# Kernel tuning notes

Hardware: AMD Instinct MI355X
Metric: run time of the kernel (lower is better)

## Reference

```python
import jax, jax.numpy as jnp
import numpy as np

N_A, N_C, N_L = 50000, 10000, 10000
HID = 128


def _gatv2(x_src, x_dst, src, dst, ea, Wl, bl, Wr, br, We, att, bias, H):
    # GATv2Conv (PyG) bipartite, edge_dim=1, concat=False (mean over heads), eval mode (no dropout)
    C = bias.shape[0]
    n_dst = x_dst.shape[0]
    xl = (x_src @ Wl + bl).reshape(-1, H, C)      # [N_src, H, C]
    xr = (x_dst @ Wr + br).reshape(-1, H, C)      # [N_dst, H, C]
    e = jax.nn.leaky_relu(xl[src] + xr[dst] + (ea @ We).reshape(-1, H, C), 0.2)  # [E,H,C]
    logit = jnp.einsum('ehc,hc->eh', e, att)      # [E,H]
    m = jax.ops.segment_max(logit, dst, num_segments=n_dst)
    m = jax.lax.stop_gradient(jnp.where(jnp.isfinite(m), m, 0.0))
    ex = jnp.exp(logit - m[dst])
    denom = jax.ops.segment_sum(ex, dst, num_segments=n_dst)
    alpha = ex / (denom[dst] + 1e-16)             # segment softmax over incoming edges
    out = jax.ops.segment_sum(alpha[:, :, None] * xl[src], dst, num_segments=n_dst)
    return out.mean(axis=1) + bias                # concat=False -> head mean + bias


def setup_inputs() -> dict:
    key = jax.random.key(0)
    ks = iter(jax.random.split(key, 80))
    def rn(shape, s=1.0):
        return jax.random.normal(next(ks), shape, jnp.float32) * s
    inp = {}
    inp['x_asset'] = rn((N_A, 512))
    inp['x_creator'] = rn((N_C, 2))
    inp['x_licensee'] = rn((N_L, 1))
    # edges: (name, E, src_max, dst_max)
    edges = [('cb', 50000, N_A, N_C), ('lt', 100000, N_A, N_L), ('sim', 200000, N_A, N_A),
             ('fw', 100000, N_A, N_A), ('rcb', 50000, N_C, N_A), ('rlt', 100000, N_L, N_A)]
    for name, E, smax, dmax in edges:
        inp[f'{name}_src'] = jax.random.randint(next(ks), (E,), 0, smax, jnp.int32)
        inp[f'{name}_dst'] = jax.random.randint(next(ks), (E,), 0, dmax, jnp.int32)
        inp[f'ea_{name}'] = rn((E, 1))
    w = 0.05  # param scale
    inp['Wp_a'] = rn((512, HID), w); inp['bp_a'] = rn((HID,), w)
    inp['Wp_c'] = rn((2, HID), w);   inp['bp_c'] = rn((HID,), w)
    inp['Wp_l'] = rn((1, HID), w);   inp['bp_l'] = rn((HID,), w)
    # layer 1: heads=2, stacked over the 6 relations
    H1 = 2
    inp['Wl1'] = rn((6, HID, H1 * HID), w); inp['bl1'] = rn((6, H1 * HID), w)
    inp['Wr1'] = rn((6, HID, H1 * HID), w); inp['br1'] = rn((6, H1 * HID), w)
    inp['We1'] = rn((6, 1, H1 * HID), w)
    inp['att1'] = rn((6, H1, HID), w); inp['bias1'] = rn((6, HID), w)
    # layer 2: heads=1
    inp['Wl2'] = rn((6, HID, HID), w); inp['bl2'] = rn((6, HID), w)
    inp['Wr2'] = rn((6, HID, HID), w); inp['br2'] = rn((6, HID), w)
    inp['We2'] = rn((6, 1, HID), w)
    inp['att2'] = rn((6, 1, HID), w); inp['bias2'] = rn((6, HID), w)
    inp['Wc1'] = rn((HID, HID), w); inp['bc1'] = rn((HID,), w)
    inp['Wc2'] = rn((HID, 3), w);   inp['bc2'] = rn((3,), w)
    inp['query_asset_index'] = 123
    return inp


def reference(x_asset, x_creator, x_licensee, Wp_a, bp_a, Wp_c, bp_c, Wp_l, bp_l,
              Wl1, bl1, Wr1, br1, We1, att1, bias1,
              Wl2, bl2, Wr2, br2, We2, att2, bias2,
              Wc1, bc1, Wc2, bc2,
              ea_cb, ea_lt, ea_sim, ea_fw, ea_rcb, ea_rlt,
              cb_src, cb_dst, lt_src, lt_dst, sim_src, sim_dst,
              fw_src, fw_dst, rcb_src, rcb_dst, rlt_src, rlt_dst,
              query_asset_index):
    x = {'Asset': x_asset @ Wp_a + bp_a,
         'Creator': x_creator @ Wp_c + bp_c,
         'Licensee': x_licensee @ Wp_l + bp_l}
    rels = [('Asset', 'Creator', cb_src, cb_dst, ea_cb),
            ('Asset', 'Licensee', lt_src, lt_dst, ea_lt),
            ('Asset', 'Asset', sim_src, sim_dst, ea_sim),
            ('Asset', 'Asset', fw_src, fw_dst, ea_fw),
            ('Creator', 'Asset', rcb_src, rcb_dst, ea_rcb),
            ('Licensee', 'Asset', rlt_src, rlt_dst, ea_rlt)]

    def hetero_layer(x, Wl, bl, Wr, br, We, att, bias, H):
        out = {k: jnp.zeros((v.shape[0], HID), v.dtype) for k, v in x.items()}
        for i, (st, dt, s, d, ea) in enumerate(rels):  # HeteroConv aggr='sum'
            out[dt] = out[dt] + _gatv2(x[st], x[dt], s, d, ea,
                                       Wl[i], bl[i], Wr[i], br[i], We[i], att[i], bias[i], H)
        return out

    x = hetero_layer(x, Wl1, bl1, Wr1, br1, We1, att1, bias1, 2)
    x = {k: jax.nn.relu(v) for k, v in x.items()}  # eval: dropout is identity
    x = hetero_layer(x, Wl2, bl2, Wr2, br2, We2, att2, bias2, 1)
    x = {k: jax.nn.relu(v) for k, v in x.items()}
    a = x['Asset'][query_asset_index]
    return jax.nn.relu(a @ Wc1 + bc1) @ Wc2 + bc2
```

## Files before the change

### kernel.cpp

```cpp
#include <hip/hip_runtime.h>
#include <math.h>

#define FAMAX 64
#define FCMAX 32
#define FLMAX 32
#define PAMAX 256
#define PCMAX 64
#define PLMAX 64
#define N1MAX 512
#define N2MAX 128

struct Inputs {
  const float *x_asset, *x_creator, *x_licensee;
  const float *Wp_a,*bp_a,*Wp_c,*bp_c,*Wp_l,*bp_l;
  const float *Wl1,*bl1,*Wr1,*br1,*We1,*att1,*bias1;
  const float *Wl2,*bl2,*Wr2,*br2,*We2,*att2,*bias2;
  const float *Wc1,*bc1,*Wc2,*bc2;
};

struct Edges {
  const int *cb_s,*cb_d;  const float* ea_cb;  int Ecb;
  const int *lt_s,*lt_d;  const float* ea_lt;  int Elt;
  const int *sim_s,*sim_d;const float* ea_sim; int Esim;
  const int *fw_s,*fw_d;  const float* ea_fw;  int Efw;
  const int *rcb_s,*rcb_d;const float* ea_rcb; int Ercb;
  const int *rlt_s,*rlt_d;const float* ea_rlt; int Erlt;
};

struct WSP {
  int* cnt;
  int *dfA,*dfC,*dfL;
  int *pfA,*pfC,*pfL;
  int *fa,*fc,*fl;
  int *pa,*pc,*pl;
  int* l2rel; int* l2src; float* l2ea;
  int* l1rel; int* l1src; int* l1dslot; float* l1ea;
  float *h0a,*h0c,*h0l;
  float *xr1a,*xr1c,*xr1l;
  float* xl1e;
  float* logit1;
  float *x1a,*x1c,*x1l;
  float* xr2q;
  float* xl2e;
  float* logit2;
};

__device__ __forceinline__ float leaky(float x){ return x > 0.f ? x : 0.2f*x; }

__device__ __forceinline__ void claim(int* flag, int* cnt, int* list, int node, int cap){
  int old = atomicCAS(&flag[node], 0, 1);
  if (old == 0){
    int k = atomicAdd(cnt, 1);
    if (k < cap){ list[k] = node; atomicExch(&flag[node], k + 2); }
    else atomicExch(&flag[node], 0);
  }
}

__global__ void k1_scan_l2(Edges eg, const int* qptr, WSP w){
  int q = qptr[0];
  if (blockIdx.x==0 && threadIdx.x==0){
    claim(w.dfA, &w.cnt[1], w.fa, q, FAMAX);
    claim(w.pfA, &w.cnt[5], w.pa, q, PAMAX);
  }
  int total = eg.Esim + eg.Efw + eg.Ercb + eg.Erlt;
  for (int i = blockIdx.x*blockDim.x + threadIdx.x; i < total; i += gridDim.x*blockDim.x){
    int j = i, rel; const int *sp,*dp; const float* ep;
    if (j < eg.Esim){ rel=2; sp=eg.sim_s; dp=eg.sim_d; ep=eg.ea_sim; }
    else { j -= eg.Esim;
      if (j < eg.Efw){ rel=3; sp=eg.fw_s; dp=eg.fw_d; ep=eg.ea_fw; }
      else { j -= eg.Efw;
        if (j < eg.Ercb){ rel=4; sp=eg.rcb_s; dp=eg.rcb_d; ep=eg.ea_rcb; }
        else { j -= eg.Ercb; rel=5; sp=eg.rlt_s; dp=eg.rlt_d; ep=eg.ea_rlt; }
      }
    }
    if (dp[j] == q){
      int src = sp[j];
      int k = atomicAdd(&w.cnt[0], 1);
      if (k < N2MAX){ w.l2rel[k]=rel; w.l2src[k]=src; w.l2ea[k]=ep[j]; }
      if (rel <= 3){ claim(w.dfA,&w.cnt[1],w.fa,src,FAMAX); claim(w.pfA,&w.cnt[5],w.pa,src,PAMAX); }
      else if (rel == 4){ claim(w.dfC,&w.cnt[2],w.fc,src,FCMAX); claim(w.pfC,&w.cnt[6],w.pc,src,PCMAX); }
      else { claim(w.dfL,&w.cnt[3],w.fl,src,FLMAX); claim(w.pfL,&w.cnt[7],w.pl,src,PLMAX); }
    }
  }
}

__global__ void k2_scan_l1(Edges eg, WSP w){
  int total = eg.Ecb+eg.Elt+eg.Esim+eg.Efw+eg.Ercb+eg.Erlt;
  for (int i = blockIdx.x*blockDim.x + threadIdx.x; i < total; i += gridDim.x*blockDim.x){
    int j = i, rel; const int *sp,*dp; const float* ep; const int* flag;
    if (j < eg.Ecb){ rel=0; sp=eg.cb_s; dp=eg.cb_d; ep=eg.ea_cb; flag=w.dfC; }
    else { j -= eg.Ecb;
    if (j < eg.Elt){ rel=1; sp=eg.lt_s; dp=eg.lt_d; ep=eg.ea_lt; flag=w.dfL; }
    else { j -= eg.Elt;
    if (j < eg.Esim){ rel=2; sp=eg.sim_s; dp=eg.sim_d; ep=eg.ea_sim; flag=w.dfA; }
    else { j -= eg.Esim;
    if (j < eg.Efw){ rel=3; sp=eg.fw_s; dp=eg.fw_d; ep=eg.ea_fw; flag=w.dfA; }
    else { j -= eg.Efw;
    if (j < eg.Ercb){ rel=4; sp=eg.rcb_s; dp=eg.rcb_d; ep=eg.ea_rcb; flag=w.dfA; }
    else { j -= eg.Ercb; rel=5; sp=eg.rlt_s; dp=eg.rlt_d; ep=eg.ea_rlt; flag=w.dfA; }}}}}
    int f = flag[dp[j]];
    if (f >= 2){
      int src = sp[j];
      int k = atomicAdd(&w.cnt[4], 1);
      if (k < N1MAX){ w.l1rel[k]=rel; w.l1src[k]=src; w.l1dslot[k]=f-2; w.l1ea[k]=ep[j]; }
      if (rel <= 3) claim(w.pfA,&w.cnt[5],w.pa,src,PAMAX);
      else if (rel == 4) claim(w.pfC,&w.cnt[6],w.pc,src,PCMAX);
      else claim(w.pfL,&w.cnt[7],w.pl,src,PLMAX);
    }
  }
}

__global__ void k3a_proj(Inputs in, WSP w){
  int b = blockIdx.x, t = threadIdx.x;
  if (b < PAMAX){
    __shared__ float xs[512];
    __shared__ float part[512];
    int npa = w.cnt[5] < PAMAX ? w.cnt[5] : PAMAX;
    if (b >= npa) return;
    int node = w.pa[b];
    xs[t] = in.x_asset[(size_t)node*512 + t];
    __syncthreads();
    int j = t & 127, g = t >> 7;
    float acc = 0.f;
    const float* W = in.Wp_a + (size_t)g*128*128 + j;
    const float* xg = xs + g*128;
    for (int k=0;k<128;k++) acc = fmaf(xg[k], W[(size_t)k*128], acc);
    part[t] = acc;
    __syncthreads();
    if (t < 128)
      w.h0a[(size_t)b*128 + t] = in.bp_a[t] + part[t] + part[128+t] + part[256+t] + part[384+t];
  } else if (b == PAMAX){
    int npc = w.cnt[6] < PCMAX ? w.cnt[6] : PCMAX;
    int j = t & 127, s0 = t >> 7;
    for (int s = s0; s < npc; s += 4){
      int node = w.pc[s];
      w.h0c[s*128 + j] = in.bp_c[j] + in.x_creator[node*2]*in.Wp_c[j]
                       + in.x_creator[node*2+1]*in.Wp_c[128+j];
    }
  } else {
    int npl = w.cnt[7] < PLMAX ? w.cnt[7] : PLMAX;
    int j = t & 127, s0 = t >> 7;
    for (int s = s0; s < npl; s += 4){
      int node = w.pl[s];
      w.h0l[s*128 + j] = in.bp_l[j] + in.x_licensee[node]*in.Wp_l[j];
    }
  }
}

__global__ void k3b_xr1(Inputs in, WSP w){
  __shared__ float h0[128];
  int b = blockIdx.x, t = threadIdx.x;
  int rel; const float* hsrc; float* dst;
  if (b < FAMAX*4){
    int slot = b >> 2, ridx = b & 3;
    int nfa = w.cnt[1] < FAMAX ? w.cnt[1] : FAMAX;
    if (slot >= nfa) return;
    rel = 2 + ridx;
    int ps = w.pfA[w.fa[slot]] - 2; if (ps < 0) return;
    hsrc = w.h0a + (size_t)ps*128;
    dst = w.xr1a + ((size_t)slot*4 + ridx)*256;
  } else if (b < FAMAX*4 + FCMAX){
    int slot = b - FAMAX*4;
    int nfc = w.cnt[2] < FCMAX ? w.cnt[2] : FCMAX;
    if (slot >= nfc) return;
    rel = 0;
    int ps = w.pfC[w.fc[slot]] - 2; if (ps < 0) return;
    hsrc = w.h0c + (size_t)ps*128;
    dst = w.xr1c + (size_t)slot*256;
  } else {
    int slot = b - FAMAX*4 - FCMAX;
    int nfl = w.cnt[3] < FLMAX ? w.cnt[3] : FLMAX;
    if (slot >= nfl) return;
    rel = 1;
    int ps = w.pfL[w.fl[slot]] - 2; if (ps < 0) return;
    hsrc = w.h0l + (size_t)ps*128;
    dst = w.xr1l + (size_t)slot*256;
  }
  if (t < 128) h0[t] = hsrc[t];
  __syncthreads();
  float acc = in.br1[rel*256 + t];
  const float* W = in.Wr1 + (size_t)rel*128*256 + t;
  for (int c=0;c<128;c++) acc = fmaf(h0[c], W[(size_t)c*256], acc);
  dst[t] = acc;
}

__global__ void k3c_edge(Inputs in, WSP w){
  __shared__ float h0[128];
  __shared__ float red[256];
  int i = blockIdx.x, t = threadIdx.x;
  int n1 = w.cnt[4] < N1MAX ? w.cnt[4] : N1MAX;
  if (i >= n1) return;
  int rel = w.l1rel[i], src = w.l1src[i], dslot = w.l1dslot[i];
  float ea = w.l1ea[i];
  int ps; const float* hsrc;
  if (rel <= 3){ ps = w.pfA[src]-2; hsrc = w.h0a + (size_t)(ps>0?ps:0)*128; }
  else if (rel == 4){ ps = w.pfC[src]-2; hsrc = w.h0c + (size_t)(ps>0?ps:0)*128; }
  else { ps = w.pfL[src]-2; hsrc = w.h0l + (size_t)(ps>0?ps:0)*128; }
  if (ps < 0){
    w.xl1e[(size_t)i*256 + t] = 0.f;
    if (t < 2) w.logit1[i*2 + t] = -INFINITY;
    return;
  }
  if (t < 128) h0[t] = hsrc[t];
  __syncthreads();
  float acc = in.bl1[rel*256 + t];
  const float* W = in.Wl1 + (size_t)rel*128*256 + t;
  for (int c=0;c<128;c++) acc = fmaf(h0[c], W[(size_t)c*256], acc);
  w.xl1e[(size_t)i*256 + t] = acc;
  const float* xr;
  if (rel >= 2) xr = w.xr1a + ((size_t)dslot*4 + (rel-2))*256;
  else if (rel == 0) xr = w.xr1c + (size_t)dslot*256;
  else xr = w.xr1l + (size_t)dslot*256;
  int h = t >> 7, c = t & 127;
  float e = leaky(acc + xr[t] + ea*in.We1[rel*256 + t]);
  red[t] = e * in.att1[(rel*2 + h)*128 + c];
  __syncthreads();
  for (int s=64; s>0; s>>=1){ if (c < s) red[t] += red[t+s]; __syncthreads(); }
  if (c == 0) w.logit1[i*2 + h] = red[t];
}

__global__ void k4_agg(Inputs in, WSP w){
  int b = blockIdx.x, j = threadIdx.x;
  int nfa = w.cnt[1] < FAMAX ? w.cnt[1] : FAMAX;
  int nfc = w.cnt[2] < FCMAX ? w.cnt[2] : FCMAX;
  int nfl = w.cnt[3] < FLMAX ? w.cnt[3] : FLMAX;
  int type, slot;
  if (b < FAMAX){ slot=b; if (slot>=nfa) return; type=0; }
  else if (b < FAMAX+FCMAX){ slot=b-FAMAX; if (slot>=nfc) return; type=1; }
  else { slot=b-FAMAX-FCMAX; if (slot>=nfl) return; type=2; }
  int n1 = w.cnt[4] < N1MAX ? w.cnt[4] : N1MAX;
  float out = 0.f;
  int r0, r1;
  if (type==0){ r0=2; r1=5; } else if (type==1){ r0=0; r1=0; } else { r0=1; r1=1; }
  for (int r=r0; r<=r1; r++){
    out += in.bias1[r*128 + j];
    float m0=-INFINITY, m1=-INFINITY;
    for (int i=0;i<n1;i++){
      if (w.l1rel[i]==r && w.l1dslot[i]==slot){
        m0 = fmaxf(m0, w.logit1[i*2]);
        m1 = fmaxf(m1, w.logit1[i*2+1]);
      }
    }
    if (m0 == -INFINITY) continue;
    float d0=0.f, d1=0.f, a0=0.f, a1=0.f;
    for (int i=0;i<n1;i++){
      if (w.l1rel[i]==r && w.l1dslot[i]==slot){
        float e0 = expf(w.logit1[i*2]   - m0);
        float e1 = expf(w.logit1[i*2+1] - m1);
        d0 += e0; d1 += e1;
        a0 = fmaf(e0, w.xl1e[(size_t)i*256 + j],       a0);
        a1 = fmaf(e1, w.xl1e[(size_t)i*256 + 128 + j], a1);
      }
    }
    out += 0.5f*(a0/(d0+1e-16f) + a1/(d1+1e-16f));
  }
  float v = fmaxf(out, 0.f);
  if (type==0) w.x1a[slot*128 + j] = v;
  else if (type==1) w.x1c[slot*128 + j] = v;
  else w.x1l[slot*128 + j] = v;
}

__global__ void k5a_xr2(Inputs in, WSP w, const int* qptr){
  __shared__ float xq[128];
  int t = threadIdx.x;
  int q = qptr[0];
  int qs = w.dfA[q] - 2;
  if (t < 128) xq[t] = w.x1a[(size_t)qs*128 + t];
  __syncthreads();
  int ridx = t >> 7, j = t & 127;
  int r = 2 + ridx;
  float acc = in.br2[r*128 + j];
  const float* W = in.Wr2 + (size_t)r*128*128 + j;
  for (int c=0;c<128;c++) acc = fmaf(xq[c], W[(size_t)c*128], acc);
  w.xr2q[ridx*128 + j] = acc;
}

__global__ void k5b_l2edge(Inputs in, WSP w){
  __shared__ float xs[128];
  __shared__ float red[128];
  int i = blockIdx.x, j = threadIdx.x;
  int n2 = w.cnt[0] < N2MAX ? w.cnt[0] : N2MAX;
  if (i >= n2) return;
  int rel = w.l2rel[i], src = w.l2src[i];
  float ea = w.l2ea[i];
  int f; const float* xb;
  if (rel <= 3){ f = w.dfA[src]; xb = w.x1a; }
  else if (rel == 4){ f = w.dfC[src]; xb = w.x1c; }
  else { f = w.dfL[src]; xb = w.x1l; }
  if (f < 2){
    w.xl2e[(size_t)i*128 + j] = 0.f;
    if (j == 0) w.logit2[i] = -INFINITY;
    return;
  }
  xs[j] = xb[(size_t)(f-2)*128 + j];
  __syncthreads();
  float acc = in.bl2[rel*128 + j];
  const float* W = in.Wl2 + (size_t)rel*128*128 + j;
  for (int c=0;c<128;c++) acc = fmaf(xs[c], W[(size_t)c*128], acc);
  w.xl2e[(size_t)i*128 + j] = acc;
  float e = leaky(acc + w.xr2q[(rel-2)*128 + j] + ea*in.We2[rel*128 + j]);
  red[j] = e * in.att2[rel*128 + j];
  __syncthreads();
  for (int s=64; s>0; s>>=1){ if (j < s) red[j] += red[j+s]; __syncthreads(); }
  if (j == 0) w.logit2[i] = red[0];
}

__global__ void k5c_final(Inputs in, WSP w, float* outp){
  __shared__ float x2[128];
  __shared__ float tt[128];
  int j = threadIdx.x;
  int n2 = w.cnt[0] < N2MAX ? w.cnt[0] : N2MAX;
  float o = 0.f;
  for (int r=2; r<=5; r++){
    o += in.bias2[r*128 + j];
    float m = -INFINITY;
    for (int i=0;i<n2;i++) if (w.l2rel[i]==r) m = fmaxf(m, w.logit2[i]);
    if (m == -INFINITY) continue;
    float d = 0.f, acc = 0.f;
    for (int i=0;i<n2;i++) if (w.l2rel[i]==r){
      float e = expf(w.logit2[i] - m);
      d += e;
      acc = fmaf(e, w.xl2e[(size_t)i*128 + j], acc);
    }
    o += acc/(d + 1e-16f);
  }
  x2[j] = fmaxf(o, 0.f);
  __syncthreads();
  float acc = in.bc1[j];
  for (int c=0;c<128;c++) acc = fmaf(x2[c], in.Wc1[c*128 + j], acc);
  tt[j] = fmaxf(acc, 0.f);
  __syncthreads();
  if (j < 3){
    float r = in.bc2[j];
    for (int c=0;c<128;c++) r = fmaf(tt[c], in.Wc2[c*3 + j], r);
    outp[j] = r;
  }
}

extern "C" void kernel_launch(void* const* d_in, const int* in_sizes, int n_in,
                              void* d_out, int out_size, void* d_ws, size_t ws_size,
                              hipStream_t stream){
  Inputs in;
  in.x_asset   = (const float*)d_in[0];
  in.x_creator = (const float*)d_in[1];
  in.x_licensee= (const float*)d_in[2];
  Edges eg;
  eg.cb_s =(const int*)d_in[3];  eg.cb_d =(const int*)d_in[4];  eg.ea_cb =(const float*)d_in[5];  eg.Ecb = in_sizes[3];
  eg.lt_s =(const int*)d_in[6];  eg.lt_d =(const int*)d_in[7];  eg.ea_lt =(const float*)d_in[8];  eg.Elt = in_sizes[6];
  eg.sim_s=(const int*)d_in[9];  eg.sim_d=(const int*)d_in[10]; eg.ea_sim=(const float*)d_in[11]; eg.Esim= in_sizes[9];
  eg.fw_s =(const int*)d_in[12]; eg.fw_d =(const int*)d_in[13]; eg.ea_fw =(const float*)d_in[14]; eg.Efw = in_sizes[12];
  eg.rcb_s=(const int*)d_in[15]; eg.rcb_d=(const int*)d_in[16]; eg.ea_rcb=(const float*)d_in[17]; eg.Ercb= in_sizes[15];
  eg.rlt_s=(const int*)d_in[18]; eg.rlt_d=(const int*)d_in[19]; eg.ea_rlt=(const float*)d_in[20]; eg.Erlt= in_sizes[18];
  in.Wp_a=(const float*)d_in[21]; in.bp_a=(const float*)d_in[22];
  in.Wp_c=(const float*)d_in[23]; in.bp_c=(const float*)d_in[24];
  in.Wp_l=(const float*)d_in[25]; in.bp_l=(const float*)d_in[26];
  in.Wl1=(const float*)d_in[27]; in.bl1=(const float*)d_in[28];
  in.Wr1=(const float*)d_in[29]; in.br1=(const float*)d_in[30];
  in.We1=(const float*)d_in[31]; in.att1=(const float*)d_in[32]; in.bias1=(const float*)d_in[33];
  in.Wl2=(const float*)d_in[34]; in.bl2=(const float*)d_in[35];
  in.Wr2=(const float*)d_in[36]; in.br2=(const float*)d_in[37];
  in.We2=(const float*)d_in[38]; in.att2=(const float*)d_in[39]; in.bias2=(const float*)d_in[40];
  in.Wc1=(const float*)d_in[41]; in.bc1=(const float*)d_in[42];
  in.Wc2=(const float*)d_in[43]; in.bc2=(const float*)d_in[44];
  const int* qptr = (const int*)d_in[45];

  char* p = (char*)d_ws;
  auto carve = [&](size_t n)->char*{ char* r = p; p += ((n + 255) & ~(size_t)255); return r; };
  WSP w;
  w.cnt  = (int*)carve(16*4);
  w.dfA  = (int*)carve(50000*4); w.dfC = (int*)carve(10000*4); w.dfL = (int*)carve(10000*4);
  w.pfA  = (int*)carve(50000*4); w.pfC = (int*)carve(10000*4); w.pfL = (int*)carve(10000*4);
  size_t zero_bytes = (size_t)(p - (char*)d_ws);
  w.fa = (int*)carve(FAMAX*4); w.fc = (int*)carve(FCMAX*4); w.fl = (int*)carve(FLMAX*4);
  w.pa = (int*)carve(PAMAX*4); w.pc = (int*)carve(PCMAX*4); w.pl = (int*)carve(PLMAX*4);
  w.l2rel=(int*)carve(N2MAX*4); w.l2src=(int*)carve(N2MAX*4); w.l2ea=(float*)carve(N2MAX*4);
  w.l1rel=(int*)carve(N1MAX*4); w.l1src=(int*)carve(N1MAX*4); w.l1dslot=(int*)carve(N1MAX*4); w.l1ea=(float*)carve(N1MAX*4);
  w.h0a=(float*)carve((size_t)PAMAX*128*4);
  w.h0c=(float*)carve((size_t)PCMAX*128*4);
  w.h0l=(float*)carve((size_t)PLMAX*128*4);
  w.xr1a=(float*)carve((size_t)FAMAX*4*256*4);
  w.xr1c=(float*)carve((size_t)FCMAX*256*4);
  w.xr1l=(float*)carve((size_t)FLMAX*256*4);
  w.xl1e=(float*)carve((size_t)N1MAX*256*4);
  w.logit1=(float*)carve((size_t)N1MAX*2*4);
  w.x1a=(float*)carve((size_t)FAMAX*128*4);
  w.x1c=(float*)carve((size_t)FCMAX*128*4);
  w.x1l=(float*)carve((size_t)FLMAX*128*4);
  w.xr2q=(float*)carve(4*128*4);
  w.xl2e=(float*)carve((size_t)N2MAX*128*4);
  w.logit2=(float*)carve(N2MAX*4);

  hipMemsetAsync(d_ws, 0, zero_bytes, stream);

  int tE2 = eg.Esim + eg.Efw + eg.Ercb + eg.Erlt;
  k1_scan_l2<<<(tE2+255)/256, 256, 0, stream>>>(eg, qptr, w);
  int tE1 = eg.Ecb + eg.Elt + tE2;
  k2_scan_l1<<<(tE1+255)/256, 256, 0, stream>>>(eg, w);
  k3a_proj<<<PAMAX+2, 512, 0, stream>>>(in, w);
  k3b_xr1<<<FAMAX*4 + FCMAX + FLMAX, 256, 0, stream>>>(in, w);
  k3c_edge<<<N1MAX, 256, 0, stream>>>(in, w);
  k4_agg<<<FAMAX + FCMAX + FLMAX, 128, 0, stream>>>(in, w);
  k5a_xr2<<<1, 512, 0, stream>>>(in, w, qptr);
  k5b_l2edge<<<N2MAX, 128, 0, stream>>>(in, w);
  k5c_final<<<1, 128, 0, stream>>>(in, w, (float*)d_out);
}
```

Baseline: 309.6 us.

## Fuse all pipeline stages into one cooperative persistent kernel with grid syncs

Replaces the memset plus nine separate kernel launches with a single cooperative kernel of 512 blocks that runs every stage, separated by grid-wide barriers. Cross-block data is passed through relaxed agent-scope atomic loads and stores. The workspace zeroing also moves inside the kernel. The aim is to remove per-launch overhead and inter-kernel gaps in a latency-bound, tiny-work pipeline. The cost is grid.sync overhead, fixed parallelism and extra complexity; if the cooperative launch fails, the original multi-kernel path runs instead.

New measurement: 711.9 us. 2.3x slower.

```diff
diff --git a/kernel.cpp b/kernel.cpp
--- a/kernel.cpp
+++ b/kernel.cpp
@@ -1,5 +1,8 @@
 #include <hip/hip_runtime.h>
+#include <hip/hip_cooperative_groups.h>
 #include <math.h>
+
+namespace cg = cooperative_groups;
 
 #define FAMAX 64
 #define FCMAX 32
@@ -9,6 +12,10 @@
 #define PLMAX 64
 #define N1MAX 512
 #define N2MAX 128
+#define DMAX  64
+#define GRID  512
+#define BLK   256
+#define NZERO (16 + 50000 + 10000 + 10000 + 50000 + 10000 + 10000)
 
 struct Inputs {
   const float *x_asset, *x_creator, *x_licensee;
@@ -46,13 +53,346 @@
 };
 
 __device__ __forceinline__ float leaky(float x){ return x > 0.f ? x : 0.2f*x; }
+__device__ __forceinline__ int   ldi(const int* p){ return __hip_atomic_load(p, __ATOMIC_RELAXED, __HIP_MEMORY_SCOPE_AGENT); }
+__device__ __forceinline__ void  sti(int* p, int v){ __hip_atomic_store(p, v, __ATOMIC_RELAXED, __HIP_MEMORY_SCOPE_AGENT); }
+__device__ __forceinline__ float ldf(const float* p){ return __hip_atomic_load(p, __ATOMIC_RELAXED, __HIP_MEMORY_SCOPE_AGENT); }
+__device__ __forceinline__ void  stf(float* p, float v){ __hip_atomic_store(p, v, __ATOMIC_RELAXED, __HIP_MEMORY_SCOPE_AGENT); }
+__device__ __forceinline__ int   imin(int a,int b){ return a<b?a:b; }
 
 __device__ __forceinline__ void claim(int* flag, int* cnt, int* list, int node, int cap){
   int old = atomicCAS(&flag[node], 0, 1);
   if (old == 0){
     int k = atomicAdd(cnt, 1);
-    if (k < cap){ list[k] = node; atomicExch(&flag[node], k + 2); }
+    if (k < cap){ sti(list + k, node); atomicExch(&flag[node], k + 2); }
     else atomicExch(&flag[node], 0);
+  }
+}
+
+__global__ __launch_bounds__(BLK, 2)
+void mega(Inputs in, Edges eg, const int* qptr, WSP w, float* outp){
+  cg::grid_group g = cg::this_grid();
+  const int t = threadIdx.x;
+  const int gtid = blockIdx.x*BLK + t;
+  const int gstride = gridDim.x*BLK;
+
+  __shared__ float xs[512];
+  __shared__ float part[256];
+  __shared__ float h0[128];
+  __shared__ float red[256];
+  __shared__ int   lrel[N1MAX];
+  __shared__ int   lslot[N1MAX];
+  __shared__ float lea[N1MAX];
+  __shared__ float lg[DMAX][2];
+  __shared__ int   eid[DMAX];
+  __shared__ float lg2[N2MAX];
+  __shared__ int   srl2[N2MAX];
+  __shared__ float vx[128];
+
+  int* zbase = w.cnt;
+  for (int i = gtid; i < NZERO; i += gstride) sti(zbase + i, 0);
+  g.sync();
+
+  int q = qptr[0];
+  if (blockIdx.x == 0 && t == 0){
+    claim(w.dfA, &w.cnt[1], w.fa, q, FAMAX);
+    claim(w.pfA, &w.cnt[5], w.pa, q, PAMAX);
+  }
+  {
+    int total = eg.Esim + eg.Efw + eg.Ercb + eg.Erlt;
+    for (int i = gtid; i < total; i += gstride){
+      int j = i, rel; const int *sp,*dp; const float* ep;
+      if (j < eg.Esim){ rel=2; sp=eg.sim_s; dp=eg.sim_d; ep=eg.ea_sim; }
+      else { j -= eg.Esim;
+        if (j < eg.Efw){ rel=3; sp=eg.fw_s; dp=eg.fw_d; ep=eg.ea_fw; }
+        else { j -= eg.Efw;
+          if (j < eg.Ercb){ rel=4; sp=eg.rcb_s; dp=eg.rcb_d; ep=eg.ea_rcb; }
+          else { j -= eg.Ercb; rel=5; sp=eg.rlt_s; dp=eg.rlt_d; ep=eg.ea_rlt; }
+        }
+      }
+      if (dp[j] == q){
+        int src = sp[j];
+        int k = atomicAdd(&w.cnt[0], 1);
+        if (k < N2MAX){ sti(w.l2rel+k, rel); sti(w.l2src+k, src); stf(w.l2ea+k, ep[j]); }
+        if (rel <= 3){ claim(w.dfA,&w.cnt[1],w.fa,src,FAMAX); claim(w.pfA,&w.cnt[5],w.pa,src,PAMAX); }
+        else if (rel == 4){ claim(w.dfC,&w.cnt[2],w.fc,src,FCMAX); claim(w.pfC,&w.cnt[6],w.pc,src,PCMAX); }
+        else { claim(w.dfL,&w.cnt[3],w.fl,src,FLMAX); claim(w.pfL,&w.cnt[7],w.pl,src,PLMAX); }
+      }
+    }
+  }
+  g.sync();
+
+  {
+    int total = eg.Ecb+eg.Elt+eg.Esim+eg.Efw+eg.Ercb+eg.Erlt;
+    for (int i = gtid; i < total; i += gstride){
+      int j = i, rel; const int *sp,*dp; const float* ep; int* flag;
+      if (j < eg.Ecb){ rel=0; sp=eg.cb_s; dp=eg.cb_d; ep=eg.ea_cb; flag=w.dfC; }
+      else { j -= eg.Ecb;
+      if (j < eg.Elt){ rel=1; sp=eg.lt_s; dp=eg.lt_d; ep=eg.ea_lt; flag=w.dfL; }
+      else { j -= eg.Elt;
+      if (j < eg.Esim){ rel=2; sp=eg.sim_s; dp=eg.sim_d; ep=eg.ea_sim; flag=w.dfA; }
+      else { j -= eg.Esim;
+      if (j < eg.Efw){ rel=3; sp=eg.fw_s; dp=eg.fw_d; ep=eg.ea_fw; flag=w.dfA; }
+      else { j -= eg.Efw;
+      if (j < eg.Ercb){ rel=4; sp=eg.rcb_s; dp=eg.rcb_d; ep=eg.ea_rcb; flag=w.dfA; }
+      else { j -= eg.Ercb; rel=5; sp=eg.rlt_s; dp=eg.rlt_d; ep=eg.ea_rlt; flag=w.dfA; }}}}}
+      int f = ldi(&flag[dp[j]]);
+      if (f >= 2){
+        int src = sp[j];
+        int k = atomicAdd(&w.cnt[4], 1);
+        if (k < N1MAX){ sti(w.l1rel+k, rel); sti(w.l1src+k, src); sti(w.l1dslot+k, f-2); stf(w.l1ea+k, ep[j]); }
+        if (rel <= 3) claim(w.pfA,&w.cnt[5],w.pa,src,PAMAX);
+        else if (rel == 4) claim(w.pfC,&w.cnt[6],w.pc,src,PCMAX);
+        else claim(w.pfL,&w.cnt[7],w.pl,src,PLMAX);
+      }
+    }
+  }
+  g.sync();
+
+  {
+    int npa = imin(ldi(&w.cnt[5]), PAMAX);
+    int npc = imin(ldi(&w.cnt[6]), PCMAX);
+    int npl = imin(ldi(&w.cnt[7]), PLMAX);
+    for (int task = blockIdx.x; task < PAMAX + 2; task += gridDim.x){
+      if (task < PAMAX){
+        if (task >= npa) continue;
+        int node = ldi(w.pa + task);
+        xs[t]     = in.x_asset[(size_t)node*512 + t];
+        xs[t+256] = in.x_asset[(size_t)node*512 + t + 256];
+        __syncthreads();
+        int j = t & 127, g2 = t >> 7;
+        float acc = 0.f;
+        const float* W = in.Wp_a + (size_t)g2*256*128 + j;
+        const float* xg = xs + g2*256;
+        for (int k=0;k<256;k++) acc = fmaf(xg[k], W[(size_t)k*128], acc);
+        part[t] = acc;
+        __syncthreads();
+        if (t < 128) stf(w.h0a + (size_t)task*128 + t, in.bp_a[t] + part[t] + part[128+t]);
+        __syncthreads();
+      } else if (task == PAMAX){
+        int j = t & 127, s0 = t >> 7;
+        for (int s = s0; s < npc; s += 2){
+          int node = ldi(w.pc + s);
+          stf(w.h0c + s*128 + j, in.bp_c[j] + in.x_creator[node*2]*in.Wp_c[j]
+                                + in.x_creator[node*2+1]*in.Wp_c[128+j]);
+        }
+      } else {
+        int j = t & 127, s0 = t >> 7;
+        for (int s = s0; s < npl; s += 2){
+          int node = ldi(w.pl + s);
+          stf(w.h0l + s*128 + j, in.bp_l[j] + in.x_licensee[node]*in.Wp_l[j]);
+        }
+      }
+    }
+  }
+  g.sync();
+
+  {
+    int nfa = imin(ldi(&w.cnt[1]), FAMAX);
+    int nfc = imin(ldi(&w.cnt[2]), FCMAX);
+    int nfl = imin(ldi(&w.cnt[3]), FLMAX);
+    int n1  = imin(ldi(&w.cnt[4]), N1MAX);
+    int ntask = FAMAX*4 + FCMAX + FLMAX + n1;
+    for (int task = blockIdx.x; task < ntask; task += gridDim.x){
+      if (task < FAMAX*4 + FCMAX + FLMAX){
+        int rel; const float* hsrc; float* dst;
+        if (task < FAMAX*4){
+          int slot = task >> 2, ridx = task & 3;
+          if (slot >= nfa) continue;
+          rel = 2 + ridx;
+          int ps = ldi(&w.pfA[ldi(w.fa + slot)]) - 2; if (ps < 0) continue;
+          hsrc = w.h0a + (size_t)ps*128;
+          dst = w.xr1a + ((size_t)slot*4 + ridx)*256;
+        } else if (task < FAMAX*4 + FCMAX){
+          int slot = task - FAMAX*4;
+          if (slot >= nfc) continue;
+          rel = 0;
+          int ps = ldi(&w.pfC[ldi(w.fc + slot)]) - 2; if (ps < 0) continue;
+          hsrc = w.h0c + (size_t)ps*128;
+          dst = w.xr1c + (size_t)slot*256;
+        } else {
+          int slot = task - FAMAX*4 - FCMAX;
+          if (slot >= nfl) continue;
+          rel = 1;
+          int ps = ldi(&w.pfL[ldi(w.fl + slot)]) - 2; if (ps < 0) continue;
+          hsrc = w.h0l + (size_t)ps*128;
+          dst = w.xr1l + (size_t)slot*256;
+        }
+        if (t < 128) h0[t] = ldf(hsrc + t);
+        __syncthreads();
+        float acc = in.br1[rel*256 + t];
+        const float* W = in.Wr1 + (size_t)rel*128*256 + t;
+        for (int c=0;c<128;c++) acc = fmaf(h0[c], W[(size_t)c*256], acc);
+        stf(dst + t, acc);
+        __syncthreads();
+      } else {
+        int i = task - (FAMAX*4 + FCMAX + FLMAX);
+        int rel = ldi(w.l1rel + i), src = ldi(w.l1src + i);
+        int ps; const float* hsrc;
+        if (rel <= 3){ ps = ldi(&w.pfA[src]) - 2; hsrc = w.h0a + (size_t)(ps>0?ps:0)*128; }
+        else if (rel == 4){ ps = ldi(&w.pfC[src]) - 2; hsrc = w.h0c + (size_t)(ps>0?ps:0)*128; }
+        else { ps = ldi(&w.pfL[src]) - 2; hsrc = w.h0l + (size_t)(ps>0?ps:0)*128; }
+        if (ps < 0){ if (t == 0) sti(w.l1rel + i, -1); continue; }
+        if (t < 128) h0[t] = ldf(hsrc + t);
+        __syncthreads();
+        float acc = in.bl1[rel*256 + t];
+        const float* W = in.Wl1 + (size_t)rel*128*256 + t;
+        for (int c=0;c<128;c++) acc = fmaf(h0[c], W[(size_t)c*256], acc);
+        stf(w.xl1e + (size_t)i*256 + t, acc);
+        __syncthreads();
+      }
+    }
+  }
+  g.sync();
+
+  {
+    int nfa = imin(ldi(&w.cnt[1]), FAMAX);
+    int nfc = imin(ldi(&w.cnt[2]), FCMAX);
+    int nfl = imin(ldi(&w.cnt[3]), FLMAX);
+    int n1  = imin(ldi(&w.cnt[4]), N1MAX);
+    for (int task = blockIdx.x; task < FAMAX + FCMAX + FLMAX; task += gridDim.x){
+      int type, slot;
+      if (task < FAMAX){ slot=task; if (slot>=nfa) continue; type=0; }
+      else if (task < FAMAX+FCMAX){ slot=task-FAMAX; if (slot>=nfc) continue; type=1; }
+      else { slot=task-FAMAX-FCMAX; if (slot>=nfl) continue; type=2; }
+      for (int i = t; i < n1; i += BLK){
+        lrel[i] = ldi(w.l1rel + i); lslot[i] = ldi(w.l1dslot + i); lea[i] = ldf(w.l1ea + i);
+      }
+      __syncthreads();
+      int h = t >> 7, c = t & 127;
+      float out = 0.f;
+      int r0, r1;
+      if (type==0){ r0=2; r1=5; } else if (type==1){ r0=0; r1=0; } else { r0=1; r1=1; }
+      for (int r=r0; r<=r1; r++){
+        if (t < 128) out += in.bias1[r*128 + t];
+        const float* xrp;
+        if (r >= 2) xrp = w.xr1a + ((size_t)slot*4 + (r-2))*256;
+        else if (r == 0) xrp = w.xr1c + (size_t)slot*256;
+        else xrp = w.xr1l + (size_t)slot*256;
+        float xrv = ldf(xrp + t);
+        float wev = in.We1[r*256 + t];
+        float atv = in.att1[(r*2 + h)*128 + c];
+        int nd = 0;
+        for (int i=0;i<n1 && nd<DMAX;i++){
+          if (lrel[i]==r && lslot[i]==slot){
+            float e = leaky(ldf(w.xl1e + (size_t)i*256 + t) + xrv + lea[i]*wev);
+            red[t] = e * atv;
+            __syncthreads();
+            for (int s=64; s>0; s>>=1){ if (c < s) red[t] += red[t+s]; __syncthreads(); }
+            if (t == 0){ lg[nd][0] = red[0]; lg[nd][1] = red[128]; eid[nd] = i; }
+            __syncthreads();
+            nd++;
+          }
+        }
+        if (nd == 0) continue;
+        float m0=-INFINITY, m1=-INFINITY;
+        for (int d=0; d<nd; d++){ m0 = fmaxf(m0, lg[d][0]); m1 = fmaxf(m1, lg[d][1]); }
+        float d0=0.f, d1=0.f;
+        for (int d=0; d<nd; d++){ d0 += expf(lg[d][0]-m0); d1 += expf(lg[d][1]-m1); }
+        if (t < 128){
+          float a0=0.f, a1=0.f;
+          for (int d=0; d<nd; d++){
+            int i = eid[d];
+            a0 = fmaf(expf(lg[d][0]-m0), ldf(w.xl1e + (size_t)i*256 + t),       a0);
+            a1 = fmaf(expf(lg[d][1]-m1), ldf(w.xl1e + (size_t)i*256 + 128 + t), a1);
+          }
+          out += 0.5f*(a0/(d0+1e-16f) + a1/(d1+1e-16f));
+        }
+        __syncthreads();
+      }
+      if (t < 128){
+        float v = fmaxf(out, 0.f);
+        if (type==0) stf(w.x1a + slot*128 + t, v);
+        else if (type==1) stf(w.x1c + slot*128 + t, v);
+        else stf(w.x1l + slot*128 + t, v);
+      }
+      __syncthreads();
+    }
+  }
+  g.sync();
+
+  {
+    int n2 = imin(ldi(&w.cnt[0]), N2MAX);
+    for (int task = blockIdx.x; task < 1 + n2; task += gridDim.x){
+      if (task == 0){
+        int qs = ldi(&w.dfA[q]) - 2;
+        if (t < 128) h0[t] = ldf(w.x1a + (size_t)qs*128 + t);
+        __syncthreads();
+        int j = t & 127;
+        for (int rr = t >> 7; rr < 4; rr += 2){
+          int r = 2 + rr;
+          float acc = in.br2[r*128 + j];
+          const float* W = in.Wr2 + (size_t)r*128*128 + j;
+          for (int c=0;c<128;c++) acc = fmaf(h0[c], W[(size_t)c*128], acc);
+          stf(w.xr2q + rr*128 + j, acc);
+        }
+        __syncthreads();
+      } else {
+        int i = task - 1;
+        int rel = ldi(w.l2rel + i), src = ldi(w.l2src + i);
+        int f; const float* xb;
+        if (rel <= 3){ f = ldi(&w.dfA[src]); xb = w.x1a; }
+        else if (rel == 4){ f = ldi(&w.dfC[src]); xb = w.x1c; }
+        else { f = ldi(&w.dfL[src]); xb = w.x1l; }
+        if (f < 2){ if (t == 0) sti(w.l2rel + i, -1); continue; }
+        if (t < 128) h0[t] = ldf(xb + (size_t)(f-2)*128 + t);
+        __syncthreads();
+        if (t < 128){
+          float acc = in.bl2[rel*128 + t];
+          const float* W = in.Wl2 + (size_t)rel*128*128 + t;
+          for (int c=0;c<128;c++) acc = fmaf(h0[c], W[(size_t)c*128], acc);
+          stf(w.xl2e + (size_t)i*128 + t, acc);
+        }
+        __syncthreads();
+      }
+    }
+  }
+  g.sync();
+
+  if (blockIdx.x == 0){
+    int n2 = imin(ldi(&w.cnt[0]), N2MAX);
+    for (int i=0;i<n2;i++){
+      int rel = ldi(w.l2rel + i);
+      if (rel < 0){ if (t == 0) srl2[i] = -1; __syncthreads(); continue; }
+      float ea = ldf(w.l2ea + i);
+      if (t < 128){
+        float e = leaky(ldf(w.xl2e + (size_t)i*128 + t) + ldf(w.xr2q + (rel-2)*128 + t)
+                        + ea*in.We2[rel*128 + t]);
+        red[t] = e * in.att2[rel*128 + t];
+      }
+      __syncthreads();
+      for (int s=64; s>0; s>>=1){ if (t < s) red[t] += red[t+s]; __syncthreads(); }
+      if (t == 0){ lg2[i] = red[0]; srl2[i] = rel; }
+      __syncthreads();
+    }
+    float o = 0.f;
+    if (t < 128){
+      for (int r=2; r<=5; r++){
+        o += in.bias2[r*128 + t];
+        float m = -INFINITY;
+        for (int i=0;i<n2;i++) if (srl2[i]==r) m = fmaxf(m, lg2[i]);
+        if (m == -INFINITY) continue;
+        float d = 0.f, acc = 0.f;
+        for (int i=0;i<n2;i++) if (srl2[i]==r){
+          float e = expf(lg2[i] - m);
+          d += e;
+          acc = fmaf(e, ldf(w.xl2e + (size_t)i*128 + t), acc);
+        }
+        o += acc/(d + 1e-16f);
+      }
+      vx[t] = fmaxf(o, 0.f);
+    }
+    __syncthreads();
+    if (t < 128){
+      float acc = in.bc1[t];
+      for (int c=0;c<128;c++) acc = fmaf(vx[c], in.Wc1[c*128 + t], acc);
+      red[t] = fmaxf(acc, 0.f);
+    }
+    __syncthreads();
+    if (t < 3){
+      float r = in.bc2[t];
+      for (int c=0;c<128;c++) r = fmaf(red[c], in.Wc2[c*3 + t], r);
+      outp[t] = r;
+    }
   }
 }
 
@@ -390,17 +730,23 @@
   w.xl2e=(float*)carve((size_t)N2MAX*128*4);
   w.logit2=(float*)carve(N2MAX*4);
 
-  hipMemsetAsync(d_ws, 0, zero_bytes, stream);
-
-  int tE2 = eg.Esim + eg.Efw + eg.Ercb + eg.Erlt;
-  k1_scan_l2<<<(tE2+255)/256, 256, 0, stream>>>(eg, qptr, w);
-  int tE1 = eg.Ecb + eg.Elt + tE2;
-  k2_scan_l1<<<(tE1+255)/256, 256, 0, stream>>>(eg, w);
-  k3a_proj<<<PAMAX+2, 512, 0, stream>>>(in, w);
-  k3b_xr1<<<FAMAX*4 + FCMAX + FLMAX, 256, 0, stream>>>(in, w);
-  k3c_edge<<<N1MAX, 256, 0, stream>>>(in, w);
-  k4_agg<<<FAMAX + FCMAX + FLMAX, 128, 0, stream>>>(in, w);
-  k5a_xr2<<<1, 512, 0, stream>>>(in, w, qptr);
-  k5b_l2edge<<<N2MAX, 128, 0, stream>>>(in, w);
-  k5c_final<<<1, 128, 0, stream>>>(in, w, (float*)d_out);
-}
+  float* outp = (float*)d_out;
+  void* args[] = { (void*)&in, (void*)&eg, (void*)&qptr, (void*)&w, (void*)&outp };
+  hipError_t err = hipLaunchCooperativeKernel((const void*)mega, dim3(GRID), dim3(BLK),
+                                              args, 0, stream);
+  if (err != hipSuccess){
+    (void)hipGetLastError();
+    hipMemsetAsync(d_ws, 0, zero_bytes, stream);
+    int tE2 = eg.Esim + eg.Efw + eg.Ercb + eg.Erlt;
+    k1_scan_l2<<<(tE2+255)/256, 256, 0, stream>>>(eg, qptr, w);
+    int tE1 = eg.Ecb + eg.Elt + tE2;
+    k2_scan_l1<<<(tE1+255)/256, 256, 0, stream>>>(eg, w);
+    k3a_proj<<<PAMAX+2, 512, 0, stream>>>(in, w);
+    k3b_xr1<<<FAMAX*4 + FCMAX + FLMAX, 256, 0, stream>>>(in, w);
+    k3c_edge<<<N1MAX, 256, 0, stream>>>(in, w);
+    k4_agg<<<FAMAX + FCMAX + FLMAX, 128, 0, stream>>>(in, w);
+    k5a_xr2<<<1, 512, 0, stream>>>(in, w, qptr);
+    k5b_l2edge<<<N2MAX, 128, 0, stream>>>(in, w);
+    k5c_final<<<1, 128, 0, stream>>>(in, w, (float*)d_out);
+  }
+}
```
